# Performance work log

Hardware: AMD Instinct MI355X
Metric: run time of the kernel (lower is better)

Reference implementation:

```python
import jax, jax.numpy as jnp
import numpy as np

L, H, P = 32768, 256, 256
DT_MIN, DT_MAX = 0.001, 0.1


def setup_inputs() -> dict:
    key = jax.random.key(0)
    ks = jax.random.split(key, 7)
    signal = jax.random.normal(ks[0], (L, H), jnp.float32)
    # stable HiPPO-like init: negative real part, random imaginary part
    lam_re = -(0.1 + 0.4 * jax.random.uniform(ks[1], (P,), jnp.float32))
    lam_im = jax.random.normal(ks[2], (P,), jnp.float32)
    Lambda_ri = jnp.stack([lam_re, lam_im], axis=-1)            # (P, 2)
    B_ri = jax.random.normal(ks[3], (P, H, 2), jnp.float32) / np.float32(np.sqrt(H))
    C_ri = jax.random.normal(ks[4], (H, P, 2), jnp.float32) / np.float32(np.sqrt(P))
    D = jax.random.uniform(ks[5], (H,), jnp.float32)
    log_step = jnp.log(DT_MIN + (DT_MAX - DT_MIN) * jax.random.uniform(ks[6], (P,), jnp.float32))
    return {"signal": signal, "Lambda_ri": Lambda_ri, "B_ri": B_ri,
            "C_ri": C_ri, "D": D, "log_step": log_step}


def reference(signal, Lambda_ri, B_ri, C_ri, D, log_step):
    # --- get_BC_tilde (bcInit='dense'): B stored real (P,H,2) -> complex ---
    Lambda = jax.lax.complex(Lambda_ri[..., 0], Lambda_ri[..., 1])   # (P,)
    B_tilde = jax.lax.complex(B_ri[..., 0], B_ri[..., 1])            # (P, H)
    C_tilde = jax.lax.complex(C_ri[..., 0], C_ri[..., 1])            # (H, P)

    # --- discretize_zoh ---
    step = jnp.exp(log_step)                                          # (P,) step_scale = 1.0
    Lambda_bar = jnp.exp(Lambda * step)                               # (P,) complex
    B_bar = ((Lambda_bar - 1.0) / Lambda)[:, None] * B_tilde          # (P, H) complex

    # --- apply_ssm: Bu_elements = vmap(u -> B_bar @ u) over time ---
    Bu = signal.astype(Lambda_bar.dtype) @ B_bar.T                    # (L, P) complex
    Lam = jnp.broadcast_to(Lambda_bar, Bu.shape)                      # (L, P)

    def binop(qi, qj):
        A_i, Bu_i = qi
        A_j, Bu_j = qj
        return (A_j * A_i, Bu_j + A_j * Bu_i)

    _, xs = jax.lax.associative_scan(binop, (Lam, Bu), axis=0)        # (L, P)

    # y = Re(C_tilde @ x) + D * u, vectorized over time
    y = jnp.real(xs @ C_tilde.T) + D * signal                         # (L, H)
    return y
```

## Files before the change

### kernel.cpp

```cpp
#include <hip/hip_runtime.h>
#include <math.h>

constexpr int L = 32768;
constexpr int H = 256;
constexpr int P = 256;
constexpr int T = 64;
constexpr int NC = L / T;
constexpr int N1 = 2 * P;
constexpr int LDEP = 130;

typedef __attribute__((ext_vector_type(8))) short short8;
typedef __attribute__((ext_vector_type(4))) float f32x4;

__device__ __forceinline__ unsigned f2bf(float f) {
  unsigned u = __float_as_uint(f);
  return (u + 0x7FFFu + ((u >> 16) & 1u)) >> 16;
}
__device__ __forceinline__ float bf_lo(unsigned u) { return __uint_as_float(u << 16); }
__device__ __forceinline__ float bf_hi(unsigned u) { return __uint_as_float(u & 0xFFFF0000u); }

__device__ __forceinline__ void gload_lds16(const unsigned short* g, unsigned short* l) {
  __builtin_amdgcn_global_load_lds(
      (const __attribute__((address_space(1))) unsigned int*)(g),
      (__attribute__((address_space(3))) unsigned int*)(l), 16, 0, 0);
}

#define KBAR(N) do { \
    asm volatile("s_waitcnt vmcnt(" #N ") lgkmcnt(0)" ::: "memory"); \
    __builtin_amdgcn_s_barrier(); \
    __builtin_amdgcn_sched_barrier(0); \
  } while (0)

#define VMEM_FENCE() __builtin_amdgcn_sched_barrier(0x38F)

__device__ __forceinline__ void lambda_bar_of(const float* __restrict__ lam,
                                              const float* __restrict__ lstep,
                                              int p, float& lbr, float& lbi) {
  float lr = lam[2 * p], li = lam[2 * p + 1];
  float st = expf(lstep[p]);
  float ea = expf(lr * st);
  lbr = ea * cosf(li * st);
  lbi = ea * sinf(li * st);
}

__global__ __launch_bounds__(256) void k_prep(const float* __restrict__ sig,
                                              const float* __restrict__ lam,
                                              const float* __restrict__ lstep,
                                              const float* __restrict__ Bri,
                                              const float* __restrict__ Cri,
                                              unsigned short* __restrict__ Bcat,
                                              unsigned short* __restrict__ Ccat,
                                              float* __restrict__ powr,
                                              float* __restrict__ powi,
                                              unsigned short* __restrict__ sigt) {
  int idx = blockIdx.x * 256 + threadIdx.x;
  if (idx < N1 * H) {
    int n = idx >> 8, k = idx & 255;
    int p = n >> 1, comp = n & 1;
    float lr = lam[2 * p], li = lam[2 * p + 1];
    float st = expf(lstep[p]);
    float ea = expf(lr * st);
    float lbr = ea * cosf(li * st), lbi = ea * sinf(li * st);
    float inv = 1.0f / (lr * lr + li * li);
    float nr = lbr - 1.0f;
    float fr = (nr * lr + lbi * li) * inv;
    float fi = (lbi * lr - nr * li) * inv;
    float br = Bri[2 * (p * H + k)], bi = Bri[2 * (p * H + k) + 1];
    float v = (comp == 0) ? (fr * br - fi * bi) : (fr * bi + fi * br);
    Bcat[idx] = (unsigned short)f2bf(v);
  } else if (idx < 2 * N1 * H) {
    int j = idx - N1 * H;
    int h = j >> 9, k2 = j & 511;
    int p = k2 >> 1;
    float v = ((k2 & 1) == 0) ? Cri[2 * (h * P + p)] : -Cri[2 * (h * P + p) + 1];
    Ccat[j] = (unsigned short)f2bf(v);
  } else if (idx < 2 * N1 * H + T * P) {
    int r = idx - 2 * N1 * H;
    int t = r >> 8, p = r & 255;
    float lr = lam[2 * p], li = lam[2 * p + 1];
    float st = expf(lstep[p]);
    float e = (float)(t + 1);
    float er = expf(e * lr * st);
    powr[r] = er * cosf(e * li * st);
    powi[r] = er * sinf(e * li * st);
  } else {
    int C = idx - (2 * N1 * H + T * P);
    int panel = C >> 12;
    int ks = (C >> 9) & 7;
    int c = C & 511;
    int row = ((c >> 8) << 6) + (((c >> 6) & 3) << 4) + (c & 15);
    int kk = ((c >> 4) & 3) << 3;
    const float* s = sig + (size_t)(panel * 128 + row) * 256 + ks * 32 + kk;
    float4 a = *(const float4*)(s);
    float4 b = *(const float4*)(s + 4);
    uint4 w;
    w.x = f2bf(a.x) | (f2bf(a.y) << 16);
    w.y = f2bf(a.z) | (f2bf(a.w) << 16);
    w.z = f2bf(b.x) | (f2bf(b.y) << 16);
    w.w = f2bf(b.z) | (f2bf(b.w) << 16);
    *(uint4*)(sigt + (size_t)C * 8) = w;
  }
}

__global__ __launch_bounds__(256, 4) void k_gemm1s(const unsigned short* __restrict__ sigt,
                                                   const unsigned short* __restrict__ Bcat,
                                                   const float* __restrict__ lam,
                                                   const float* __restrict__ lstep,
                                                   unsigned short* __restrict__ Xl,
                                                   float* __restrict__ Sr,
                                                   float* __restrict__ Si) {
  constexpr int NIT = 8;
  __shared__ __align__(16) char smem[40960];
  unsigned short* sA[3] = {(unsigned short*)smem, (unsigned short*)(smem + 8192),
                           (unsigned short*)(smem + 16384)};
  unsigned short* sB[2] = {(unsigned short*)(smem + 24576), (unsigned short*)(smem + 32768)};
  float* sEpi = (float*)smem;
  const int tid = threadIdx.x;
  const int lane = tid & 63;
  const int wave = tid >> 6;
  const int wc = (wave & 1) * 64;
  const int m0 = blockIdx.x * 128, n0 = blockIdx.y * 128;
  const int brow = ((tid >> 6) << 4) | (tid & 15);
  const int bko = ((tid >> 4) & 3) * 8;
  const int hb = (wave & 1) * 2048;
  const int afb = (wave >> 1) * 256;
  const unsigned short* apan = sigt + (size_t)blockIdx.x * 32768;
  f32x4 acc[4][4];
#pragma unroll
  for (int i = 0; i < 4; i++)
#pragma unroll
    for (int j = 0; j < 4; j++) acc[i][j] = (f32x4){0.f, 0.f, 0.f, 0.f};

#define ISSUE_A1(ks, buf) { \
    gload_lds16(apan + (ks) * 4096 + tid * 8, sA[buf] + tid * 8); \
    gload_lds16(apan + (ks) * 4096 + 2048 + tid * 8, sA[buf] + 2048 + tid * 8); }
#define ISSUE_B1(ks, buf) { \
    gload_lds16(Bcat + (size_t)(n0 + brow) * 256 + (ks) * 32 + bko, sB[buf] + tid * 8); \
    gload_lds16(Bcat + (size_t)(n0 + 64 + brow) * 256 + (ks) * 32 + bko, sB[buf] + 2048 + tid * 8); }

  ISSUE_A1(0, 0);
  VMEM_FENCE();
  ISSUE_B1(0, 0);
  VMEM_FENCE();
  ISSUE_A1(1, 1);
  VMEM_FENCE();
  KBAR(2);
#pragma unroll
  for (int it = 0; it < NIT; it++) {
    if (it + 1 < NIT) ISSUE_B1(it + 1, (it + 1) & 1);
    VMEM_FENCE();
    if (it + 2 < NIT) ISSUE_A1(it + 2, (it + 2) % 3);
    VMEM_FENCE();
    const unsigned short* sAc = sA[it % 3];
    const unsigned short* sBc = sB[it & 1];
    short8 af[4], bfr[4];
#pragma unroll
    for (int i = 0; i < 4; i++) af[i] = *(const short8*)(sAc + (afb + i * 64 + lane) * 8);
#pragma unroll
    for (int j = 0; j < 4; j++) bfr[j] = *(const short8*)(sBc + hb + (j * 64 + lane) * 8);
#pragma unroll
    for (int i = 0; i < 4; i++)
#pragma unroll
      for (int j = 0; j < 4; j++)
        acc[i][j] = __builtin_amdgcn_mfma_f32_16x16x32_bf16(af[i], bfr[j], acc[i][j], 0, 0, 0);
    if (it + 1 < NIT) {
      if (it + 2 < NIT) { KBAR(2); } else { KBAR(0); }
    }
  }
  __syncthreads();

  const int crow = (lane >> 4) * 4, ccol = wc + (lane & 15);
#pragma unroll
  for (int half = 0; half < 2; half++) {
    if ((wave >> 1) == half) {
#pragma unroll
      for (int i = 0; i < 4; i++)
#pragma unroll
        for (int j = 0; j < 4; j++)
#pragma unroll
          for (int g = 0; g < 4; g++)
            sEpi[(crow + i * 16 + g) * LDEP + ccol + j * 16] = acc[i][j][g];
    }
    __syncthreads();
    if (tid < 64) {
      const int pl = tid;
      const int gp = (n0 >> 1) + pl;
      const int c = blockIdx.x * 2 + half;
      float lbr, lbi;
      lambda_bar_of(lam, lstep, gp, lbr, lbi);
      float xr = 0.f, xi = 0.f;
      const float* e = sEpi + 2 * pl;
      const size_t gbase = (size_t)(m0 + half * 64) * N1 + n0 + 2 * pl;
      for (int tb = 0; tb < T; tb += 8) {
        float2 v[8];
#pragma unroll
        for (int u = 0; u < 8; u++) v[u] = *(const float2*)(e + (tb + u) * LDEP);
        unsigned ov[8];
#pragma unroll
        for (int u = 0; u < 8; u++) {
          float nr = fmaf(lbr, xr, fmaf(-lbi, xi, v[u].x));
          float ni = fmaf(lbr, xi, fmaf(lbi, xr, v[u].y));
          xr = nr; xi = ni;
          ov[u] = f2bf(xr) | (f2bf(xi) << 16);
        }
#pragma unroll
        for (int u = 0; u < 8; u++)
          *(unsigned*)(Xl + gbase + (size_t)(tb + u) * N1) = ov[u];
      }
      Sr[(size_t)gp * NC + c] = xr;
      Si[(size_t)gp * NC + c] = xi;
    }
    __syncthreads();
  }
#undef ISSUE_A1
#undef ISSUE_B1
}

__global__ __launch_bounds__(64) void k_carry2(const float* __restrict__ lam,
                                               const float* __restrict__ lstep,
                                               const float* __restrict__ Sr,
                                               const float* __restrict__ Si,
                                               float* __restrict__ car, float* __restrict__ cai) {
  const int p = blockIdx.x;
  const int t = threadIdx.x;
  float lr = lam[2 * p], li = lam[2 * p + 1];
  float st = expf(lstep[p]);
  float eT = expf((float)T * lr * st);
  float lTr = eT * cosf((float)T * li * st);
  float lTi = eT * sinf((float)T * li * st);
  float vr[8], vi[8];
  {
    const float* srp = Sr + (size_t)p * NC + t * 8;
    const float* sip = Si + (size_t)p * NC + t * 8;
    float4 a0 = *(const float4*)(srp), a1 = *(const float4*)(srp + 4);
    float4 b0 = *(const float4*)(sip), b1 = *(const float4*)(sip + 4);
    vr[0] = a0.x; vr[1] = a0.y; vr[2] = a0.z; vr[3] = a0.w;
    vr[4] = a1.x; vr[5] = a1.y; vr[6] = a1.z; vr[7] = a1.w;
    vi[0] = b0.x; vi[1] = b0.y; vi[2] = b0.z; vi[3] = b0.w;
    vi[4] = b1.x; vi[5] = b1.y; vi[6] = b1.z; vi[7] = b1.w;
  }
  float Br = 0.f, Bi = 0.f;
#pragma unroll
  for (int u = 0; u < 8; u++) {
    float nr = fmaf(lTr, Br, fmaf(-lTi, Bi, vr[u]));
    float ni = fmaf(lTr, Bi, fmaf(lTi, Br, vi[u]));
    Br = nr; Bi = ni;
  }
  float e8 = expf(8.0f * (float)T * lr * st);
  float Ar = e8 * cosf(8.0f * (float)T * li * st);
  float Ai = e8 * sinf(8.0f * (float)T * li * st);
#pragma unroll
  for (int d = 1; d < 64; d <<= 1) {
    float Aor = __shfl_up(Ar, d), Aoi = __shfl_up(Ai, d);
    float Bor = __shfl_up(Br, d), Boi = __shfl_up(Bi, d);
    if (t >= d) {
      float nBr = Ar * Bor - Ai * Boi + Br;
      float nBi = Ar * Boi + Ai * Bor + Bi;
      float nAr = Aor * Ar - Aoi * Ai;
      float nAi = Aor * Ai + Aoi * Ar;
      Br = nBr; Bi = nBi; Ar = nAr; Ai = nAi;
    }
  }
  float cr = __shfl_up(Br, 1), ci = __shfl_up(Bi, 1);
  if (t == 0) { cr = 0.f; ci = 0.f; }
#pragma unroll
  for (int u = 0; u < 8; u++) {
    car[(t * 8 + u) * P + p] = cr;
    cai[(t * 8 + u) * P + p] = ci;
    float nr = fmaf(lTr, cr, fmaf(-lTi, ci, vr[u]));
    float ni = fmaf(lTr, ci, fmaf(lTi, cr, vi[u]));
    cr = nr; ci = ni;
  }
}

__device__ __forceinline__ unsigned mix1(unsigned u, float pr, float pi, float cr, float ci) {
  float re = bf_lo(u) + (pr * cr - pi * ci);
  float im = bf_hi(u) + (pr * ci + pi * cr);
  return f2bf(re) | (f2bf(im) << 16);
}

__global__ __launch_bounds__(256) void k_fix(const unsigned short* __restrict__ Xl,
                                             const float* __restrict__ powr,
                                             const float* __restrict__ powi,
                                             const float* __restrict__ car,
                                             const float* __restrict__ cai,
                                             unsigned short* __restrict__ Xg) {
  int g = blockIdx.x * 256 + threadIdx.x;
  int row = g >> 4, seg = g & 15;
  int t = row & 63, cidx = row >> 6, rowp = row & 127, panel = row >> 7;
  int p0 = seg * 16;
  const unsigned short* xs = Xl + (size_t)row * N1 + seg * 32;
  uint4 x0 = *(const uint4*)(xs);
  uint4 x1 = *(const uint4*)(xs + 8);
  uint4 x2 = *(const uint4*)(xs + 16);
  uint4 x3 = *(const uint4*)(xs + 24);
  const float* prB = powr + t * P + p0;
  const float* piB = powi + t * P + p0;
  const float* crB = car + cidx * P + p0;
  const float* ciB = cai + cidx * P + p0;
  const int cb = ((rowp >> 6) << 8) | (((rowp >> 4) & 3) << 6) | (rowp & 15);
  unsigned short* xd = Xg + (size_t)panel * 65536 + (size_t)seg * 4096 + cb * 8;
#define FIXQ(XQ, q) { \
    float4 pr = *(const float4*)(prB + 4 * (q)); \
    float4 pi = *(const float4*)(piB + 4 * (q)); \
    float4 cr = *(const float4*)(crB + 4 * (q)); \
    float4 ci = *(const float4*)(ciB + 4 * (q)); \
    uint4 o; \
    o.x = mix1(XQ.x, pr.x, pi.x, cr.x, ci.x); \
    o.y = mix1(XQ.y, pr.y, pi.y, cr.y, ci.y); \
    o.z = mix1(XQ.z, pr.z, pi.z, cr.z, ci.z); \
    o.w = mix1(XQ.w, pr.w, pi.w, cr.w, ci.w); \
    *(uint4*)(xd + (q) * 128) = o; }
  FIXQ(x0, 0);
  FIXQ(x1, 1);
  FIXQ(x2, 2);
  FIXQ(x3, 3);
#undef FIXQ
}

__global__ __launch_bounds__(256, 4) void k_gemm2p(const unsigned short* __restrict__ Xg,
                                                   const unsigned short* __restrict__ Ccat,
                                                   const float* __restrict__ sig,
                                                   const float* __restrict__ Dv,
                                                   float* __restrict__ out) {
  constexpr int NIT = 16;
  __shared__ __align__(16) char smem[32768];
  unsigned short* sA[3] = {(unsigned short*)smem, (unsigned short*)(smem + 8192),
                           (unsigned short*)(smem + 16384)};
  unsigned short* sB[2] = {(unsigned short*)(smem + 24576), (unsigned short*)(smem + 28672)};
  const int tid = threadIdx.x;
  const int lane = tid & 63;
  const int wave = tid >> 6;
  const int m0 = blockIdx.x * 128, n0 = blockIdx.y * 64;
  const int brow = (((tid >> 6) & 3) << 4) | (tid & 15);
  const int bko = ((tid >> 4) & 3) * 8;
  const int afb = (wave >> 1) * 256;
  const int bfb = (wave & 1) * 2;
  const unsigned short* apan = Xg + (size_t)blockIdx.x * 65536;
  f32x4 acc[4][2];
#pragma unroll
  for (int i = 0; i < 4; i++)
#pragma unroll
    for (int j = 0; j < 2; j++) acc[i][j] = (f32x4){0.f, 0.f, 0.f, 0.f};

#define ISSUE_A2(ks, buf) { \
    gload_lds16(apan + (ks) * 4096 + tid * 8, sA[buf] + tid * 8); \
    gload_lds16(apan + (ks) * 4096 + 2048 + tid * 8, sA[buf] + 2048 + tid * 8); }
#define ISSUE_B2(ks, buf) { \
    gload_lds16(Ccat + (size_t)(n0 + brow) * 512 + (ks) * 32 + bko, sB[buf] + tid * 8); }

  ISSUE_A2(0, 0);
  VMEM_FENCE();
  ISSUE_B2(0, 0);
  VMEM_FENCE();
  ISSUE_A2(1, 1);
  VMEM_FENCE();
  KBAR(2);
#pragma unroll
  for (int it = 0; it < NIT; it++) {
    if (it + 1 < NIT) ISSUE_B2(it + 1, (it + 1) & 1);
    VMEM_FENCE();
    if (it + 2 < NIT) ISSUE_A2(it + 2, (it + 2) % 3);
    VMEM_FENCE();
    const unsigned short* sAc = sA[it % 3];
    const unsigned short* sBc = sB[it & 1];
    short8 af[4], bfr[2];
#pragma unroll
    for (int i = 0; i < 4; i++) af[i] = *(const short8*)(sAc + (afb + i * 64 + lane) * 8);
#pragma unroll
    for (int j = 0; j < 2; j++) bfr[j] = *(const short8*)(sBc + ((bfb + j) * 64 + lane) * 8);
#pragma unroll
    for (int i = 0; i < 4; i++)
#pragma unroll
      for (int j = 0; j < 2; j++)
        acc[i][j] = __builtin_amdgcn_mfma_f32_16x16x32_bf16(af[i], bfr[j], acc[i][j], 0, 0, 0);
    if (it + 1 < NIT) {
      if (it + 2 < NIT) { KBAR(2); } else { KBAR(0); }
    }
  }

  const int crow = (wave >> 1) * 64 + (lane >> 4) * 4;
  const int ccol = (wave & 1) * 32 + (lane & 15);
  float dcol[2];
#pragma unroll
  for (int j = 0; j < 2; j++) dcol[j] = Dv[n0 + ccol + j * 16];
#pragma unroll
  for (int i = 0; i < 4; i++)
#pragma unroll
    for (int j = 0; j < 2; j++) {
      int col = n0 + ccol + j * 16;
#pragma unroll
      for (int g = 0; g < 4; g++) {
        int row = m0 + crow + i * 16 + g;
        out[(size_t)row * H + col] = acc[i][j][g] + dcol[j] * sig[(size_t)row * H + col];
      }
    }
#undef ISSUE_A2
#undef ISSUE_B2
}

extern "C" void kernel_launch(void* const* d_in, const int* in_sizes, int n_in,
                              void* d_out, int out_size, void* d_ws, size_t ws_size,
                              hipStream_t stream) {
  const float* sig = (const float*)d_in[0];
  const float* lam = (const float*)d_in[1];
  const float* Bri = (const float*)d_in[2];
  const float* Cri = (const float*)d_in[3];
  const float* Dv  = (const float*)d_in[4];
  const float* lst = (const float*)d_in[5];
  float* out = (float*)d_out;

  unsigned short* Bcat = (unsigned short*)d_ws;
  unsigned short* Ccat = Bcat + (size_t)N1 * H;
  unsigned short* Xl   = Ccat + (size_t)H * N1;
  float* powr = (float*)(Xl + (size_t)L * N1);
  float* powi = powr + T * P;
  float* Sr   = powi + T * P;
  float* Si   = Sr + NC * P;
  float* car  = Si + NC * P;
  float* cai  = car + NC * P;
  unsigned short* sigt = (unsigned short*)(cai + NC * P);
  unsigned short* Xg   = sigt + (size_t)L * H;

  k_prep<<<(2 * N1 * H + T * P + L * H / 8) / 256, 256, 0, stream>>>(
      sig, lam, lst, Bri, Cri, Bcat, Ccat, powr, powi, sigt);
  dim3 g1(L / 128, N1 / 128);
  k_gemm1s<<<g1, 256, 0, stream>>>(sigt, Bcat, lam, lst, Xl, Sr, Si);
  k_carry2<<<NC / 2, 64, 0, stream>>>(lam, lst, Sr, Si, car, cai);
  k_fix<<<L * 16 / 256, 256, 0, stream>>>(Xl, powr, powi, car, cai, Xg);
  dim3 g2(L / 128, H / 64);
  k_gemm2p<<<g2, 256, 0, stream>>>(Xg, Ccat, sig, Dv, out);
}
```

Measured before the change: 156.5 us.

## Fold chunk-carry correction into output GEMM as extra K-dimension

Removes the separate fix-up kernel that added carry*power terms to the local scan states and rewrote them in GEMM-friendly layout. The first GEMM now writes local states directly in the tiled panel layout, and the output GEMM doubles its K loop: the second half builds A tiles on the fly from power and carry products (packed to bf16 in LDS) and multiplies them against the same C tiles. This drops a full read/write pass over the large state buffer and one launch, in exchange for extra MFMA work and register-computed staging in the second GEMM. The carry kernel launch now uses P blocks.

```diff
diff --git a/kernel.cpp b/kernel.cpp
--- a/kernel.cpp
+++ b/kernel.cpp
@@ -16,8 +16,6 @@
   unsigned u = __float_as_uint(f);
   return (u + 0x7FFFu + ((u >> 16) & 1u)) >> 16;
 }
-__device__ __forceinline__ float bf_lo(unsigned u) { return __uint_as_float(u << 16); }
-__device__ __forceinline__ float bf_hi(unsigned u) { return __uint_as_float(u & 0xFFFF0000u); }
 
 __device__ __forceinline__ void gload_lds16(const unsigned short* g, unsigned short* l) {
   __builtin_amdgcn_global_load_lds(
@@ -43,6 +41,12 @@
   lbi = ea * sinf(li * st);
 }
 
+__device__ __forceinline__ unsigned pkcm(float ar, float ai, float br, float bi) {
+  float re = ar * br - ai * bi;
+  float im = fmaf(ar, bi, ai * br);
+  return f2bf(re) | (f2bf(im) << 16);
+}
+
 __global__ __launch_bounds__(256) void k_prep(const float* __restrict__ sig,
                                               const float* __restrict__ lam,
                                               const float* __restrict__ lstep,
@@ -50,8 +54,7 @@
                                               const float* __restrict__ Cri,
                                               unsigned short* __restrict__ Bcat,
                                               unsigned short* __restrict__ Ccat,
-                                              float* __restrict__ powr,
-                                              float* __restrict__ powi,
+                                              float* __restrict__ powc,
                                               unsigned short* __restrict__ sigt) {
   int idx = blockIdx.x * 256 + threadIdx.x;
   if (idx < N1 * H) {
@@ -81,8 +84,8 @@
     float st = expf(lstep[p]);
     float e = (float)(t + 1);
     float er = expf(e * lr * st);
-    powr[r] = er * cosf(e * li * st);
-    powi[r] = er * sinf(e * li * st);
+    powc[2 * r] = er * cosf(e * li * st);
+    powc[2 * r + 1] = er * sinf(e * li * st);
   } else {
     int C = idx - (2 * N1 * H + T * P);
     int panel = C >> 12;
@@ -119,7 +122,7 @@
   const int lane = tid & 63;
   const int wave = tid >> 6;
   const int wc = (wave & 1) * 64;
-  const int m0 = blockIdx.x * 128, n0 = blockIdx.y * 128;
+  const int n0 = blockIdx.y * 128;
   const int brow = ((tid >> 6) << 4) | (tid & 15);
   const int bko = ((tid >> 4) & 3) * 8;
   const int hb = (wave & 1) * 2048;
@@ -190,7 +193,9 @@
       lambda_bar_of(lam, lstep, gp, lbr, lbi);
       float xr = 0.f, xi = 0.f;
       const float* e = sEpi + 2 * pl;
-      const size_t gbase = (size_t)(m0 + half * 64) * N1 + n0 + 2 * pl;
+      const int ks = blockIdx.y * 4 + (pl >> 4);
+      const int kkb = (pl >> 2) & 3;
+      unsigned short* xlb = Xl + (size_t)blockIdx.x * 65536 + ks * 4096 + 2 * (pl & 3);
       for (int tb = 0; tb < T; tb += 8) {
         float2 v[8];
 #pragma unroll
@@ -203,9 +208,10 @@
           xr = nr; xi = ni;
           ov[u] = f2bf(xr) | (f2bf(xi) << 16);
         }
+        const int cb0 = (half << 8) | (((tb >> 4) & 3) << 6) | (kkb << 4) | (tb & 15);
 #pragma unroll
         for (int u = 0; u < 8; u++)
-          *(unsigned*)(Xl + gbase + (size_t)(tb + u) * N1) = ov[u];
+          *(unsigned*)(xlb + (cb0 + u) * 8) = ov[u];
       }
       Sr[(size_t)gp * NC + c] = xr;
       Si[(size_t)gp * NC + c] = xi;
@@ -220,7 +226,7 @@
                                                const float* __restrict__ lstep,
                                                const float* __restrict__ Sr,
                                                const float* __restrict__ Si,
-                                               float* __restrict__ car, float* __restrict__ cai) {
+                                               float* __restrict__ carc) {
   const int p = blockIdx.x;
   const int t = threadIdx.x;
   float lr = lam[2 * p], li = lam[2 * p + 1];
@@ -265,65 +271,22 @@
   if (t == 0) { cr = 0.f; ci = 0.f; }
 #pragma unroll
   for (int u = 0; u < 8; u++) {
-    car[(t * 8 + u) * P + p] = cr;
-    cai[(t * 8 + u) * P + p] = ci;
+    float2 w; w.x = cr; w.y = ci;
+    *(float2*)(carc + 2 * ((size_t)(t * 8 + u) * P + p)) = w;
     float nr = fmaf(lTr, cr, fmaf(-lTi, ci, vr[u]));
     float ni = fmaf(lTr, ci, fmaf(lTi, cr, vi[u]));
     cr = nr; ci = ni;
   }
 }
 
-__device__ __forceinline__ unsigned mix1(unsigned u, float pr, float pi, float cr, float ci) {
-  float re = bf_lo(u) + (pr * cr - pi * ci);
-  float im = bf_hi(u) + (pr * ci + pi * cr);
-  return f2bf(re) | (f2bf(im) << 16);
-}
-
-__global__ __launch_bounds__(256) void k_fix(const unsigned short* __restrict__ Xl,
-                                             const float* __restrict__ powr,
-                                             const float* __restrict__ powi,
-                                             const float* __restrict__ car,
-                                             const float* __restrict__ cai,
-                                             unsigned short* __restrict__ Xg) {
-  int g = blockIdx.x * 256 + threadIdx.x;
-  int row = g >> 4, seg = g & 15;
-  int t = row & 63, cidx = row >> 6, rowp = row & 127, panel = row >> 7;
-  int p0 = seg * 16;
-  const unsigned short* xs = Xl + (size_t)row * N1 + seg * 32;
-  uint4 x0 = *(const uint4*)(xs);
-  uint4 x1 = *(const uint4*)(xs + 8);
-  uint4 x2 = *(const uint4*)(xs + 16);
-  uint4 x3 = *(const uint4*)(xs + 24);
-  const float* prB = powr + t * P + p0;
-  const float* piB = powi + t * P + p0;
-  const float* crB = car + cidx * P + p0;
-  const float* ciB = cai + cidx * P + p0;
-  const int cb = ((rowp >> 6) << 8) | (((rowp >> 4) & 3) << 6) | (rowp & 15);
-  unsigned short* xd = Xg + (size_t)panel * 65536 + (size_t)seg * 4096 + cb * 8;
-#define FIXQ(XQ, q) { \
-    float4 pr = *(const float4*)(prB + 4 * (q)); \
-    float4 pi = *(const float4*)(piB + 4 * (q)); \
-    float4 cr = *(const float4*)(crB + 4 * (q)); \
-    float4 ci = *(const float4*)(ciB + 4 * (q)); \
-    uint4 o; \
-    o.x = mix1(XQ.x, pr.x, pi.x, cr.x, ci.x); \
-    o.y = mix1(XQ.y, pr.y, pi.y, cr.y, ci.y); \
-    o.z = mix1(XQ.z, pr.z, pi.z, cr.z, ci.z); \
-    o.w = mix1(XQ.w, pr.w, pi.w, cr.w, ci.w); \
-    *(uint4*)(xd + (q) * 128) = o; }
-  FIXQ(x0, 0);
-  FIXQ(x1, 1);
-  FIXQ(x2, 2);
-  FIXQ(x3, 3);
-#undef FIXQ
-}
-
-__global__ __launch_bounds__(256, 4) void k_gemm2p(const unsigned short* __restrict__ Xg,
+__global__ __launch_bounds__(256, 4) void k_gemm2c(const unsigned short* __restrict__ Xl,
                                                    const unsigned short* __restrict__ Ccat,
+                                                   const float* __restrict__ powc,
+                                                   const float* __restrict__ carc,
                                                    const float* __restrict__ sig,
                                                    const float* __restrict__ Dv,
                                                    float* __restrict__ out) {
-  constexpr int NIT = 16;
+  constexpr int NIT = 32;
   __shared__ __align__(16) char smem[32768];
   unsigned short* sA[3] = {(unsigned short*)smem, (unsigned short*)(smem + 8192),
                            (unsigned short*)(smem + 16384)};
@@ -336,7 +299,12 @@
   const int bko = ((tid >> 4) & 3) * 8;
   const int afb = (wave >> 1) * 256;
   const int bfb = (wave & 1) * 2;
-  const unsigned short* apan = Xg + (size_t)blockIdx.x * 65536;
+  const unsigned short* apan = Xl + (size_t)blockIdx.x * 65536;
+  const int t_ = (((tid >> 6) & 3) << 4) | (tid & 15);
+  const int kk1 = ((tid >> 4) & 3) << 3;
+  const float* pwB = powc + t_ * 512 + kk1;
+  const float* c1B = carc + (size_t)(blockIdx.x * 2) * 512 + kk1;
+  const float* c2B = c1B + 512;
   f32x4 acc[4][2];
 #pragma unroll
   for (int i = 0; i < 4; i++)
@@ -349,6 +317,25 @@
 #define ISSUE_B2(ks, buf) { \
     gload_lds16(Ccat + (size_t)(n0 + brow) * 512 + (ks) * 32 + bko, sB[buf] + tid * 8); }
 
+  float4 pa, pb, ca, cb, da, db;
+#define LOAD_T(ks) { const int ko_ = (ks) * 32; \
+    pa = *(const float4*)(pwB + ko_); pb = *(const float4*)(pwB + ko_ + 4); \
+    ca = *(const float4*)(c1B + ko_); cb = *(const float4*)(c1B + ko_ + 4); \
+    da = *(const float4*)(c2B + ko_); db = *(const float4*)(c2B + ko_ + 4); }
+#define STAGE_FIX(buf) { \
+    uint4 o1, o2; \
+    o1.x = pkcm(pa.x, pa.y, ca.x, ca.y); \
+    o1.y = pkcm(pa.z, pa.w, ca.z, ca.w); \
+    o1.z = pkcm(pb.x, pb.y, cb.x, cb.y); \
+    o1.w = pkcm(pb.z, pb.w, cb.z, cb.w); \
+    o2.x = pkcm(pa.x, pa.y, da.x, da.y); \
+    o2.y = pkcm(pa.z, pa.w, da.z, da.w); \
+    o2.z = pkcm(pb.x, pb.y, db.x, db.y); \
+    o2.w = pkcm(pb.z, pb.w, db.z, db.w); \
+    unsigned short* dA_ = sA[buf]; \
+    *(uint4*)(dA_ + tid * 8) = o1; \
+    *(uint4*)(dA_ + 2048 + tid * 8) = o2; }
+
   ISSUE_A2(0, 0);
   VMEM_FENCE();
   ISSUE_B2(0, 0);
@@ -358,10 +345,13 @@
   KBAR(2);
 #pragma unroll
   for (int it = 0; it < NIT; it++) {
-    if (it + 1 < NIT) ISSUE_B2(it + 1, (it + 1) & 1);
+    if (it >= 15 && it + 1 < NIT) LOAD_T((it + 1) & 15);
     VMEM_FENCE();
-    if (it + 2 < NIT) ISSUE_A2(it + 2, (it + 2) % 3);
+    if (it + 1 < NIT) ISSUE_B2((it + 1) & 15, (it + 1) & 1);
     VMEM_FENCE();
+    if (it + 2 < 16) ISSUE_A2(it + 2, (it + 2) % 3);
+    VMEM_FENCE();
+    if (it >= 15 && it + 1 < NIT) STAGE_FIX((it + 1) % 3);
     const unsigned short* sAc = sA[it % 3];
     const unsigned short* sBc = sB[it & 1];
     short8 af[4], bfr[2];
@@ -375,7 +365,8 @@
       for (int j = 0; j < 2; j++)
         acc[i][j] = __builtin_amdgcn_mfma_f32_16x16x32_bf16(af[i], bfr[j], acc[i][j], 0, 0, 0);
     if (it + 1 < NIT) {
-      if (it + 2 < NIT) { KBAR(2); } else { KBAR(0); }
+      if (it + 2 < 16) { KBAR(2); }
+      else { KBAR(0); }
     }
   }
 
@@ -397,6 +388,8 @@
     }
 #undef ISSUE_A2
 #undef ISSUE_B2
+#undef LOAD_T
+#undef STAGE_FIX
 }
 
 extern "C" void kernel_launch(void* const* d_in, const int* in_sizes, int n_in,
@@ -413,21 +406,17 @@
   unsigned short* Bcat = (unsigned short*)d_ws;
   unsigned short* Ccat = Bcat + (size_t)N1 * H;
   unsigned short* Xl   = Ccat + (size_t)H * N1;
-  float* powr = (float*)(Xl + (size_t)L * N1);
-  float* powi = powr + T * P;
-  float* Sr   = powi + T * P;
+  float* powc = (float*)(Xl + (size_t)L * N1);
+  float* carc = powc + 2 * T * P;
+  float* Sr   = carc + 2 * NC * P;
   float* Si   = Sr + NC * P;
-  float* car  = Si + NC * P;
-  float* cai  = car + NC * P;
-  unsigned short* sigt = (unsigned short*)(cai + NC * P);
-  unsigned short* Xg   = sigt + (size_t)L * H;
+  unsigned short* sigt = (unsigned short*)(Si + NC * P);
 
   k_prep<<<(2 * N1 * H + T * P + L * H / 8) / 256, 256, 0, stream>>>(
-      sig, lam, lst, Bri, Cri, Bcat, Ccat, powr, powi, sigt);
+      sig, lam, lst, Bri, Cri, Bcat, Ccat, powc, sigt);
   dim3 g1(L / 128, N1 / 128);
   k_gemm1s<<<g1, 256, 0, stream>>>(sigt, Bcat, lam, lst, Xl, Sr, Si);
-  k_carry2<<<NC / 2, 64, 0, stream>>>(lam, lst, Sr, Si, car, cai);
-  k_fix<<<L * 16 / 256, 256, 0, stream>>>(Xl, powr, powi, car, cai, Xg);
+  k_carry2<<<P, 64, 0, stream>>>(lam, lst, Sr, Si, carc);
   dim3 g2(L / 128, H / 64);
-  k_gemm2p<<<g2, 256, 0, stream>>>(Xg, Ccat, sig, Dv, out);
-}
+  k_gemm2c<<<g2, 256, 0, stream>>>(Xl, Ccat, powc, carc, sig, Dv, out);
+}
```

After: 171.7 us. 9.7% more time.
